# Optimization experiments

Measured on AMD Instinct MI355X. Metric: run time of the kernel, lower is better.

The kernel has to match this reference:

```python
import jax, jax.numpy as jnp
import numpy as np

N = 8192
NFEAT = 64
OUT = 64


def setup_inputs() -> dict:
    key = jax.random.key(0)
    ks = jax.random.split(key, 7)
    A_stack = jax.random.uniform(ks[0], (N, N, 5), dtype=jnp.float32)
    feature = jax.random.normal(ks[1], (N, NFEAT), dtype=jnp.float32)
    weight_b = jax.random.uniform(ks[2], (5, 1), dtype=jnp.float32) * 0.1
    stdv1 = 1.0 / np.sqrt(OUT)
    W1 = jax.random.uniform(ks[3], (NFEAT, OUT), dtype=jnp.float32, minval=-stdv1, maxval=stdv1)
    b1 = jax.random.uniform(ks[4], (OUT,), dtype=jnp.float32, minval=-stdv1, maxval=stdv1)
    W2 = jax.random.uniform(ks[5], (OUT, OUT), dtype=jnp.float32, minval=-stdv1, maxval=stdv1)
    b2 = jax.random.uniform(ks[6], (OUT,), dtype=jnp.float32, minval=-stdv1, maxval=stdv1)
    return {"A_stack": A_stack, "feature": feature, "weight_b": weight_b,
            "W1": W1, "b1": b1, "W2": W2, "b2": b2}


def reference(A_stack, feature, weight_b, W1, b1, W2, b2):
    # Multiplex relation aggregation: weighted sum of 5 adjacency layers, then symmetrize.
    temp = jnp.einsum('ijk,kl->ij', A_stack, weight_b)  # [N, N]
    final_A = temp + temp.T
    # GCN layer 1: spmm(adj, X @ W1) + b1
    U1 = final_A @ (feature @ W1) + b1
    # GCN layer 2
    U2 = final_A @ (U1 @ W2) + b2
    return (U1 + U2) * 0.5
```

## Files before the change

### kernel.cpp

```cpp
#include <hip/hip_runtime.h>
#include <hip/hip_bf16.h>


#define NN 8192

typedef __attribute__((ext_vector_type(8))) short short8;
typedef __attribute__((ext_vector_type(8))) unsigned short u16x8;
typedef __attribute__((ext_vector_type(4))) float f32x4;

static __device__ __forceinline__ unsigned short f2bf(float f) {
    unsigned u = __float_as_uint(f);
    u += 0x7FFFu + ((u >> 16) & 1u);
    return (unsigned short)(u >> 16);
}

__global__ __launch_bounds__(256) void k_sym_build(
        const float* __restrict__ A, const float* __restrict__ wb,
        unsigned short* __restrict__ S) {
    __shared__ float Tt[64 * 65];

    int b = blockIdx.x;
    double disc = 66049.0 - 8.0 * (double)b;
    int bi = (int)((257.0 - sqrt(disc)) * 0.5);
    if (bi < 0) bi = 0; if (bi > 127) bi = 127;
    while (bi < 127 && (bi + 1) * (257 - (bi + 1)) / 2 <= b) ++bi;
    while (bi > 0 && bi * (257 - bi) / 2 > b) --bi;
    int bj = bi + (b - bi * (257 - bi) / 2);

    const float w0 = wb[0], w1 = wb[1], w2 = wb[2], w3 = wb[3], w4 = wb[4];
    int t = threadIdx.x;
    int j = t & 63;
    int iw = t >> 6;

    float t1[16];
    #pragma unroll
    for (int e = 0; e < 16; ++e) {
        int i = iw + e * 4;
        const float* p = A + ((long long)(bi * 64 + i) * NN + (bj * 64 + j)) * 5;
        t1[e] = p[0]*w0 + p[1]*w1 + p[2]*w2 + p[3]*w3 + p[4]*w4;
        const float* q = A + ((long long)(bj * 64 + i) * NN + (bi * 64 + j)) * 5;
        Tt[i * 65 + j] = q[0]*w0 + q[1]*w1 + q[2]*w2 + q[3]*w3 + q[4]*w4;
    }
    __syncthreads();
    float s[16];
    #pragma unroll
    for (int e = 0; e < 16; ++e) {
        int i = iw + e * 4;
        s[e] = t1[e] + Tt[j * 65 + i];
        S[(long long)(bi * 64 + i) * NN + bj * 64 + j] = f2bf(s[e]);
    }
    __syncthreads();
    #pragma unroll
    for (int e = 0; e < 16; ++e) { int i = iw + e * 4; Tt[i * 65 + j] = s[e]; }
    __syncthreads();
    if (bi != bj) {
        #pragma unroll
        for (int e = 0; e < 16; ++e) {
            int i = iw + e * 4;
            S[(long long)(bj * 64 + i) * NN + bi * 64 + j] = f2bf(Tt[j * 65 + i]);
        }
    }
}

__global__ __launch_bounds__(256) void k_small_gemm_t(
        const float* __restrict__ X, const float* __restrict__ W,
        unsigned short* __restrict__ Yt) {
    __shared__ float Ys[64 * 65];
    int t = threadIdx.x, lane = t & 63, w = t >> 6;
    float wcol[64];
    #pragma unroll
    for (int k = 0; k < 64; ++k) wcol[k] = W[k * 64 + lane];
    int r0 = blockIdx.x * 64;
    for (int rr = 0; rr < 16; ++rr) {
        const float* x = X + (long long)(r0 + w * 16 + rr) * 64;
        float acc = 0.f;
        #pragma unroll
        for (int k = 0; k < 64; ++k) acc += x[k] * wcol[k];
        Ys[lane * 65 + w * 16 + rr] = acc;
    }
    __syncthreads();
    #pragma unroll
    for (int e = 0; e < 16; ++e) {
        int elem = t + e * 256;
        int c = elem >> 6, jj = elem & 63;
        Yt[(long long)c * NN + r0 + jj] = f2bf(Ys[c * 65 + jj]);
    }
}

template<int SRC, int FINAL>
__global__ __launch_bounds__(256) void k_gemm_skinny(
        const unsigned short* __restrict__ S,
        const float* __restrict__ A, const float* __restrict__ wb,
        const unsigned short* __restrict__ Ht,
        const float* __restrict__ bias,
        const float* __restrict__ U1,
        float* __restrict__ Y) {
    __shared__ unsigned short TsU[16 * 128];
    __shared__ unsigned short HsU[64 * 128];
    int t = threadIdx.x, lane = t & 63, w = t >> 6;
    int i0 = blockIdx.x * 16;
    f32x4 acc = {0.f, 0.f, 0.f, 0.f};

    float w0 = 0.f, w1 = 0.f, w2 = 0.f, w3 = 0.f, w4 = 0.f;
    if (SRC == 1) { w0 = wb[0]; w1 = wb[1]; w2 = wb[2]; w3 = wb[3]; w4 = wb[4]; }

    const int si = t >> 4, sjc = (t & 15) * 8;
    const int hf = t >> 2, hcc = (t & 3) * 32;
    const int row = lane & 15, kg = lane >> 4;
    const int hrow = w * 16 + row;

    for (int jt = 0; jt < NN; jt += 128) {
        __syncthreads();
        if (SRC == 0) {
            u16x8 v = *(const u16x8*)(S + (long long)(i0 + si) * NN + jt + sjc);
            *(u16x8*)((char*)TsU + (si * 256 + ((sjc * 2) ^ ((si & 7) << 4)))) = v;
        } else {
            u16x8 vout;
            #pragma unroll
            for (int q2 = 0; q2 < 8; ++q2) {
                int jj = sjc + q2;
                const float* p1 = A + ((long long)(i0 + si) * NN + jt + jj) * 5;
                const float* p2 = A + ((long long)(jt + jj) * NN + i0 + si) * 5;
                float v = p1[0]*w0 + p1[1]*w1 + p1[2]*w2 + p1[3]*w3 + p1[4]*w4
                        + p2[0]*w0 + p2[1]*w1 + p2[2]*w2 + p2[3]*w3 + p2[4]*w4;
                vout[q2] = f2bf(v);
            }
            *(u16x8*)((char*)TsU + (si * 256 + ((sjc * 2) ^ ((si & 7) << 4)))) = vout;
        }
        {
            const u16x8* hp = (const u16x8*)(Ht + (long long)hf * NN + jt + hcc);
            #pragma unroll
            for (int q = 0; q < 4; ++q) {
                u16x8 v = hp[q];
                *(u16x8*)((char*)HsU + (hf * 256 + (((hcc + q * 8) * 2) ^ ((hf & 7) << 4)))) = v;
            }
        }
        __syncthreads();
        #pragma unroll
        for (int kk = 0; kk < 4; ++kk) {
            short8 a = *(const short8*)((const char*)TsU +
                        (row * 256 + ((kk * 64 + kg * 16) ^ ((row & 7) << 4))));
            short8 bfrag = *(const short8*)((const char*)HsU +
                        (hrow * 256 + ((kk * 64 + kg * 16) ^ ((row & 7) << 4))));
            acc = __builtin_amdgcn_mfma_f32_16x16x32_bf16(a, bfrag, acc, 0, 0, 0);
        }
    }

    int r4 = lane >> 4;
    int f = w * 16 + row;
    float bv = bias[f];
    #pragma unroll
    for (int r = 0; r < 4; ++r) {
        long long i = i0 + r4 * 4 + r;
        float v = acc[r] + bv;
        if (FINAL) v = 0.5f * (U1[i * 64 + f] + v);
        Y[i * 64 + f] = v;
    }
}

extern "C" void kernel_launch(void* const* d_in, const int* in_sizes, int n_in,
                              void* d_out, int out_size, void* d_ws, size_t ws_size,
                              hipStream_t stream) {
    const float* A    = (const float*)d_in[0];
    const float* feat = (const float*)d_in[1];
    const float* wb   = (const float*)d_in[2];
    const float* W1   = (const float*)d_in[3];
    const float* b1   = (const float*)d_in[4];
    const float* W2   = (const float*)d_in[5];
    const float* b2   = (const float*)d_in[6];
    float* out = (float*)d_out;

    const size_t szS = (size_t)NN * NN * 2;
    const size_t szH = (size_t)64 * NN * 2;
    const size_t szU = (size_t)NN * 64 * 4;
    char* p = (char*)d_ws;
    bool fast = ws_size >= szS + 2 * szH + szU;

    unsigned short *S, *H1t, *H2t; float* U1;
    if (fast) {
        S   = (unsigned short*)p;
        H1t = (unsigned short*)(p + szS);
        H2t = (unsigned short*)(p + szS + szH);
        U1  = (float*)(p + szS + 2 * szH);
    } else {
        S   = nullptr;
        H1t = (unsigned short*)p;
        H2t = (unsigned short*)(p + szH);
        U1  = (float*)(p + 2 * szH);
    }

    if (fast) k_sym_build<<<8256, 256, 0, stream>>>(A, wb, S);
    k_small_gemm_t<<<128, 256, 0, stream>>>(feat, W1, H1t);
    if (fast) k_gemm_skinny<0, 0><<<512, 256, 0, stream>>>(S, A, wb, H1t, b1, nullptr, U1);
    else      k_gemm_skinny<1, 0><<<512, 256, 0, stream>>>(S, A, wb, H1t, b1, nullptr, U1);
    k_small_gemm_t<<<128, 256, 0, stream>>>(U1, W2, H2t);
    if (fast) k_gemm_skinny<0, 1><<<512, 256, 0, stream>>>(S, A, wb, H2t, b2, U1, out);
    else      k_gemm_skinny<1, 1><<<512, 256, 0, stream>>>(S, A, wb, H2t, b2, U1, out);
}
```

Baseline: 447.6 us.

## Vectorize sym build loads, split-K skinny GEMM over waves, drop fallback path

The symmetric build kernel now reads A with 16-byte nontemporal vector loads (each thread covers 4 consecutive columns of 5 floats) and writes S with 4-wide packed stores. The skinny GEMM no longer stages tiles in LDS. Each wave covers a quarter of K, reads its S and H fragments directly from global memory into four MFMA accumulators, and the partial sums are reduced through shared memory. The small GEMM gets vector loads and 8-wide transposed stores. The fallback path that rebuilt S on the fly when workspace was too small is removed, so the code now always assumes a large enough workspace.

```diff
diff --git a/kernel.cpp b/kernel.cpp
--- a/kernel.cpp
+++ b/kernel.cpp
@@ -6,6 +6,7 @@
 
 typedef __attribute__((ext_vector_type(8))) short short8;
 typedef __attribute__((ext_vector_type(8))) unsigned short u16x8;
+typedef __attribute__((ext_vector_type(4))) unsigned short u16x4;
 typedef __attribute__((ext_vector_type(4))) float f32x4;
 
 static __device__ __forceinline__ unsigned short f2bf(float f) {
@@ -29,35 +30,70 @@
 
     const float w0 = wb[0], w1 = wb[1], w2 = wb[2], w3 = wb[3], w4 = wb[4];
     int t = threadIdx.x;
-    int j = t & 63;
-    int iw = t >> 6;
-
-    float t1[16];
-    #pragma unroll
-    for (int e = 0; e < 16; ++e) {
-        int i = iw + e * 4;
-        const float* p = A + ((long long)(bi * 64 + i) * NN + (bj * 64 + j)) * 5;
-        t1[e] = p[0]*w0 + p[1]*w1 + p[2]*w2 + p[3]*w3 + p[4]*w4;
-        const float* q = A + ((long long)(bj * 64 + i) * NN + (bi * 64 + j)) * 5;
-        Tt[i * 65 + j] = q[0]*w0 + q[1]*w1 + q[2]*w2 + q[3]*w3 + q[4]*w4;
-    }
-    __syncthreads();
-    float s[16];
-    #pragma unroll
-    for (int e = 0; e < 16; ++e) {
-        int i = iw + e * 4;
-        s[e] = t1[e] + Tt[j * 65 + i];
-        S[(long long)(bi * 64 + i) * NN + bj * 64 + j] = f2bf(s[e]);
-    }
-    __syncthreads();
-    #pragma unroll
-    for (int e = 0; e < 16; ++e) { int i = iw + e * 4; Tt[i * 65 + j] = s[e]; }
+    int qc = t & 15;
+    int r0 = t >> 4;
+
+    float t1[4][4];
+    #pragma unroll
+    for (int e = 0; e < 4; ++e) {
+        int r = r0 + 16 * e;
+        {
+            const f32x4* p = (const f32x4*)(A +
+                ((long long)(bi * 64 + r) * NN + bj * 64 + 4 * qc) * 5);
+            f32x4 f0 = __builtin_nontemporal_load(p);
+            f32x4 f1 = __builtin_nontemporal_load(p + 1);
+            f32x4 f2 = __builtin_nontemporal_load(p + 2);
+            f32x4 f3 = __builtin_nontemporal_load(p + 3);
+            f32x4 f4 = __builtin_nontemporal_load(p + 4);
+            t1[e][0] = f0[0]*w0 + f0[1]*w1 + f0[2]*w2 + f0[3]*w3 + f1[0]*w4;
+            t1[e][1] = f1[1]*w0 + f1[2]*w1 + f1[3]*w2 + f2[0]*w3 + f2[1]*w4;
+            t1[e][2] = f2[2]*w0 + f2[3]*w1 + f3[0]*w2 + f3[1]*w3 + f3[2]*w4;
+            t1[e][3] = f3[3]*w0 + f4[0]*w1 + f4[1]*w2 + f4[2]*w3 + f4[3]*w4;
+        }
+        {
+            const f32x4* p = (const f32x4*)(A +
+                ((long long)(bj * 64 + r) * NN + bi * 64 + 4 * qc) * 5);
+            f32x4 f0 = __builtin_nontemporal_load(p);
+            f32x4 f1 = __builtin_nontemporal_load(p + 1);
+            f32x4 f2 = __builtin_nontemporal_load(p + 2);
+            f32x4 f3 = __builtin_nontemporal_load(p + 3);
+            f32x4 f4 = __builtin_nontemporal_load(p + 4);
+            Tt[r * 65 + 4*qc + 0] = f0[0]*w0 + f0[1]*w1 + f0[2]*w2 + f0[3]*w3 + f1[0]*w4;
+            Tt[r * 65 + 4*qc + 1] = f1[1]*w0 + f1[2]*w1 + f1[3]*w2 + f2[0]*w3 + f2[1]*w4;
+            Tt[r * 65 + 4*qc + 2] = f2[2]*w0 + f2[3]*w1 + f3[0]*w2 + f3[1]*w3 + f3[2]*w4;
+            Tt[r * 65 + 4*qc + 3] = f3[3]*w0 + f4[0]*w1 + f4[1]*w2 + f4[2]*w3 + f4[3]*w4;
+        }
+    }
+    __syncthreads();
+    float sv[4][4];
+    #pragma unroll
+    for (int e = 0; e < 4; ++e) {
+        int r = r0 + 16 * e;
+        u16x4 o;
+        #pragma unroll
+        for (int q = 0; q < 4; ++q) {
+            float v = t1[e][q] + Tt[(4*qc + q) * 65 + r];
+            sv[e][q] = v;
+            o[q] = f2bf(v);
+        }
+        *(u16x4*)(S + (long long)(bi * 64 + r) * NN + bj * 64 + 4 * qc) = o;
+    }
+    __syncthreads();
+    #pragma unroll
+    for (int e = 0; e < 4; ++e) {
+        int r = r0 + 16 * e;
+        #pragma unroll
+        for (int q = 0; q < 4; ++q) Tt[r * 65 + 4*qc + q] = sv[e][q];
+    }
     __syncthreads();
     if (bi != bj) {
         #pragma unroll
-        for (int e = 0; e < 16; ++e) {
-            int i = iw + e * 4;
-            S[(long long)(bj * 64 + i) * NN + bi * 64 + j] = f2bf(Tt[j * 65 + i]);
+        for (int e = 0; e < 4; ++e) {
+            int r = r0 + 16 * e;
+            u16x4 o;
+            #pragma unroll
+            for (int q = 0; q < 4; ++q) o[q] = f2bf(Tt[(4*qc + q) * 65 + r]);
+            *(u16x4*)(S + (long long)(bj * 64 + r) * NN + bi * 64 + 4 * qc) = o;
         }
     }
 }
@@ -72,89 +108,77 @@
     for (int k = 0; k < 64; ++k) wcol[k] = W[k * 64 + lane];
     int r0 = blockIdx.x * 64;
     for (int rr = 0; rr < 16; ++rr) {
-        const float* x = X + (long long)(r0 + w * 16 + rr) * 64;
+        const f32x4* x = (const f32x4*)(X + (long long)(r0 + w * 16 + rr) * 64);
         float acc = 0.f;
         #pragma unroll
-        for (int k = 0; k < 64; ++k) acc += x[k] * wcol[k];
+        for (int k4 = 0; k4 < 16; ++k4) {
+            f32x4 xv = x[k4];
+            acc += xv[0]*wcol[4*k4] + xv[1]*wcol[4*k4+1]
+                 + xv[2]*wcol[4*k4+2] + xv[3]*wcol[4*k4+3];
+        }
         Ys[lane * 65 + w * 16 + rr] = acc;
     }
     __syncthreads();
-    #pragma unroll
-    for (int e = 0; e < 16; ++e) {
-        int elem = t + e * 256;
-        int c = elem >> 6, jj = elem & 63;
-        Yt[(long long)c * NN + r0 + jj] = f2bf(Ys[c * 65 + jj]);
-    }
-}
-
-template<int SRC, int FINAL>
+    int c = t >> 2, j0 = (t & 3) * 16;
+    u16x8 o0, o1;
+    #pragma unroll
+    for (int q = 0; q < 8; ++q) {
+        o0[q] = f2bf(Ys[c * 65 + j0 + q]);
+        o1[q] = f2bf(Ys[c * 65 + j0 + 8 + q]);
+    }
+    *(u16x8*)(Yt + (long long)c * NN + r0 + j0) = o0;
+    *(u16x8*)(Yt + (long long)c * NN + r0 + j0 + 8) = o1;
+}
+
+template<int FINAL>
 __global__ __launch_bounds__(256) void k_gemm_skinny(
         const unsigned short* __restrict__ S,
-        const float* __restrict__ A, const float* __restrict__ wb,
         const unsigned short* __restrict__ Ht,
         const float* __restrict__ bias,
         const float* __restrict__ U1,
         float* __restrict__ Y) {
-    __shared__ unsigned short TsU[16 * 128];
-    __shared__ unsigned short HsU[64 * 128];
-    int t = threadIdx.x, lane = t & 63, w = t >> 6;
+    __shared__ float red[4][16][64];
+    int t = threadIdx.x;
+    int lane = t & 63, w = t >> 6;
     int i0 = blockIdx.x * 16;
-    f32x4 acc = {0.f, 0.f, 0.f, 0.f};
-
-    float w0 = 0.f, w1 = 0.f, w2 = 0.f, w3 = 0.f, w4 = 0.f;
-    if (SRC == 1) { w0 = wb[0]; w1 = wb[1]; w2 = wb[2]; w3 = wb[3]; w4 = wb[4]; }
-
-    const int si = t >> 4, sjc = (t & 15) * 8;
-    const int hf = t >> 2, hcc = (t & 3) * 32;
-    const int row = lane & 15, kg = lane >> 4;
-    const int hrow = w * 16 + row;
-
-    for (int jt = 0; jt < NN; jt += 128) {
-        __syncthreads();
-        if (SRC == 0) {
-            u16x8 v = *(const u16x8*)(S + (long long)(i0 + si) * NN + jt + sjc);
-            *(u16x8*)((char*)TsU + (si * 256 + ((sjc * 2) ^ ((si & 7) << 4)))) = v;
-        } else {
-            u16x8 vout;
-            #pragma unroll
-            for (int q2 = 0; q2 < 8; ++q2) {
-                int jj = sjc + q2;
-                const float* p1 = A + ((long long)(i0 + si) * NN + jt + jj) * 5;
-                const float* p2 = A + ((long long)(jt + jj) * NN + i0 + si) * 5;
-                float v = p1[0]*w0 + p1[1]*w1 + p1[2]*w2 + p1[3]*w3 + p1[4]*w4
-                        + p2[0]*w0 + p2[1]*w1 + p2[2]*w2 + p2[3]*w3 + p2[4]*w4;
-                vout[q2] = f2bf(v);
-            }
-            *(u16x8*)((char*)TsU + (si * 256 + ((sjc * 2) ^ ((si & 7) << 4)))) = vout;
-        }
-        {
-            const u16x8* hp = (const u16x8*)(Ht + (long long)hf * NN + jt + hcc);
-            #pragma unroll
-            for (int q = 0; q < 4; ++q) {
-                u16x8 v = hp[q];
-                *(u16x8*)((char*)HsU + (hf * 256 + (((hcc + q * 8) * 2) ^ ((hf & 7) << 4)))) = v;
-            }
-        }
-        __syncthreads();
+    int r = lane & 15, kg = lane >> 4;
+
+    const unsigned short* aRow = S + (long long)(i0 + r) * NN + kg * 8;
+    const unsigned short* bRow = Ht + (long long)r * NN + kg * 8;
+    f32x4 acc0 = {0,0,0,0}, acc1 = {0,0,0,0}, acc2 = {0,0,0,0}, acc3 = {0,0,0,0};
+
+    int j0 = w * 2048;
+    for (int jt = j0; jt < j0 + 2048; jt += 128) {
         #pragma unroll
         for (int kk = 0; kk < 4; ++kk) {
-            short8 a = *(const short8*)((const char*)TsU +
-                        (row * 256 + ((kk * 64 + kg * 16) ^ ((row & 7) << 4))));
-            short8 bfrag = *(const short8*)((const char*)HsU +
-                        (hrow * 256 + ((kk * 64 + kg * 16) ^ ((row & 7) << 4))));
-            acc = __builtin_amdgcn_mfma_f32_16x16x32_bf16(a, bfrag, acc, 0, 0, 0);
-        }
-    }
-
-    int r4 = lane >> 4;
-    int f = w * 16 + row;
-    float bv = bias[f];
-    #pragma unroll
-    for (int r = 0; r < 4; ++r) {
-        long long i = i0 + r4 * 4 + r;
-        float v = acc[r] + bv;
-        if (FINAL) v = 0.5f * (U1[i * 64 + f] + v);
-        Y[i * 64 + f] = v;
+            int off = jt + kk * 32;
+            short8 a   = *(const short8*)(aRow + off);
+            short8 bb0 = *(const short8*)(bRow + off);
+            short8 bb1 = *(const short8*)(bRow + 16 * NN + off);
+            short8 bb2 = *(const short8*)(bRow + 32 * NN + off);
+            short8 bb3 = *(const short8*)(bRow + 48 * NN + off);
+            acc0 = __builtin_amdgcn_mfma_f32_16x16x32_bf16(a, bb0, acc0, 0, 0, 0);
+            acc1 = __builtin_amdgcn_mfma_f32_16x16x32_bf16(a, bb1, acc1, 0, 0, 0);
+            acc2 = __builtin_amdgcn_mfma_f32_16x16x32_bf16(a, bb2, acc2, 0, 0, 0);
+            acc3 = __builtin_amdgcn_mfma_f32_16x16x32_bf16(a, bb3, acc3, 0, 0, 0);
+        }
+    }
+    #pragma unroll
+    for (int rr = 0; rr < 4; ++rr) {
+        red[w][kg * 4 + rr][r]      = acc0[rr];
+        red[w][kg * 4 + rr][16 + r] = acc1[rr];
+        red[w][kg * 4 + rr][32 + r] = acc2[rr];
+        red[w][kg * 4 + rr][48 + r] = acc3[rr];
+    }
+    __syncthreads();
+    #pragma unroll
+    for (int e = 0; e < 4; ++e) {
+        int idx = t + e * 256;
+        int m = idx >> 6, c = idx & 63;
+        float v = red[0][m][c] + red[1][m][c] + red[2][m][c] + red[3][m][c] + bias[c];
+        long long gi = (long long)(i0 + m) * 64 + c;
+        if (FINAL) v = 0.5f * (U1[gi] + v);
+        Y[gi] = v;
     }
 }
 
@@ -172,28 +196,15 @@
 
     const size_t szS = (size_t)NN * NN * 2;
     const size_t szH = (size_t)64 * NN * 2;
-    const size_t szU = (size_t)NN * 64 * 4;
     char* p = (char*)d_ws;
-    bool fast = ws_size >= szS + 2 * szH + szU;
-
-    unsigned short *S, *H1t, *H2t; float* U1;
-    if (fast) {
-        S   = (unsigned short*)p;
-        H1t = (unsigned short*)(p + szS);
-        H2t = (unsigned short*)(p + szS + szH);
-        U1  = (float*)(p + szS + 2 * szH);
-    } else {
-        S   = nullptr;
-        H1t = (unsigned short*)p;
-        H2t = (unsigned short*)(p + szH);
-        U1  = (float*)(p + 2 * szH);
-    }
-
-    if (fast) k_sym_build<<<8256, 256, 0, stream>>>(A, wb, S);
+    unsigned short* S   = (unsigned short*)p;
+    unsigned short* H1t = (unsigned short*)(p + szS);
+    unsigned short* H2t = (unsigned short*)(p + szS + szH);
+    float*          U1  = (float*)(p + szS + 2 * szH);
+
+    k_sym_build<<<8256, 256, 0, stream>>>(A, wb, S);
     k_small_gemm_t<<<128, 256, 0, stream>>>(feat, W1, H1t);
-    if (fast) k_gemm_skinny<0, 0><<<512, 256, 0, stream>>>(S, A, wb, H1t, b1, nullptr, U1);
-    else      k_gemm_skinny<1, 0><<<512, 256, 0, stream>>>(S, A, wb, H1t, b1, nullptr, U1);
+    k_gemm_skinny<0><<<512, 256, 0, stream>>>(S, H1t, b1, nullptr, U1);
     k_small_gemm_t<<<128, 256, 0, stream>>>(U1, W2, H2t);
-    if (fast) k_gemm_skinny<0, 1><<<512, 256, 0, stream>>>(S, A, wb, H2t, b2, U1, out);
-    else      k_gemm_skinny<1, 1><<<512, 256, 0, stream>>>(S, A, wb, H2t, b2, U1, out);
-}
+    k_gemm_skinny<1><<<512, 256, 0, stream>>>(S, H2t, b2, U1, out);
+}
```

Result: slower. 783.8 us (+75.1%).
